# Optimization experiments

Hardware: AMD Instinct MI355X
Metric: run time of the kernel (lower is better)

Reference implementation:

```python
import jax, jax.numpy as jnp
import numpy as np

IN_DIM = 128
OUT_DIM = 128
NUM_RELS = 8
N_NODES = 50000
N_EDGES = 500000


def setup_inputs() -> dict:
    key = jax.random.key(0)
    k_x, k_ei_s, k_ei_d, k_et, k_w, k_sw = jax.random.split(key, 6)
    x = jax.random.normal(k_x, (N_NODES, IN_DIM), dtype=jnp.float32)
    src = jax.random.randint(k_ei_s, (N_EDGES,), 0, N_NODES)
    dst = jax.random.randint(k_ei_d, (N_EDGES,), 0, N_NODES)
    edge_index = jnp.stack([src, dst], axis=0).astype(jnp.int64)
    edge_type = jax.random.randint(k_et, (N_EDGES,), 0, NUM_RELS).astype(jnp.int64)
    # xavier_uniform: bound = sqrt(6/(fan_in+fan_out))
    bw = float(np.sqrt(6.0 / (IN_DIM + OUT_DIM)))
    weight = jax.random.uniform(k_w, (NUM_RELS, IN_DIM, OUT_DIM), dtype=jnp.float32, minval=-bw, maxval=bw)
    self_loop_weight = jax.random.uniform(k_sw, (IN_DIM, OUT_DIM), dtype=jnp.float32, minval=-bw, maxval=bw)
    bias = jnp.zeros((OUT_DIM,), dtype=jnp.float32)
    return {
        "x": x,
        "weight": weight,
        "self_loop_weight": self_loop_weight,
        "bias": bias,
        "edge_index": edge_index,
        "edge_type": edge_type,
        "num_entities": N_NODES,
    }


def reference(x, weight, self_loop_weight, bias, edge_index, edge_type, num_entities):
    # Relation-grouped formulation of the per-edge loop:
    # transform every node under every relation once: hr[r, n, o]
    hr = jnp.einsum("nd,rdo->rno", x, weight)
    src, dst = edge_index[0], edge_index[1]
    # per-edge message = x[src] @ weight[edge_type]  == hr[edge_type, src]
    msg = hr[edge_type, src]  # [E, out]
    agg = jax.ops.segment_sum(msg, dst, num_segments=num_entities)  # scatter-add into out[dst]
    out = agg + x @ self_loop_weight + bias
    return jax.nn.relu(out)
```

## Files before the change

### kernel.cpp

```cpp
#include <hip/hip_runtime.h>

#define IN_DIM 128
#define OUT_DIM 128
#define NUM_RELS 8
#define SCAN_ELEMS 2048

typedef unsigned short u16;
typedef u16 u16x8 __attribute__((ext_vector_type(8)));
typedef u16 u16x4 __attribute__((ext_vector_type(4)));
typedef __bf16 bf16x8 __attribute__((ext_vector_type(8)));
typedef float f32x4 __attribute__((ext_vector_type(4)));

__device__ __forceinline__ u16 f2bf(float f) {
    unsigned u = __float_as_uint(f);
    u += 0x7FFF + ((u >> 16) & 1);
    return (u16)(u >> 16);
}
__device__ __forceinline__ float bf2f(u16 h) {
    return __uint_as_float((unsigned)h << 16);
}

__global__ __launch_bounds__(256) void k_prep(
    const float* __restrict__ x, const float* __restrict__ weight,
    const float* __restrict__ slw,
    u16* __restrict__ xb, u16* __restrict__ WbT, int* __restrict__ cursor,
    int N, int BA, int BB)
{
    const int b = blockIdx.x;
    const int tid = threadIdx.x;
    if (b < BA) {
        long i = ((long)b * 256 + tid) * 4;
        if (i < (long)N * 128) {
            float4 v = *(const float4*)(x + i);
            u16x4 o;
            o[0] = f2bf(v.x); o[1] = f2bf(v.y); o[2] = f2bf(v.z); o[3] = f2bf(v.w);
            *(u16x4*)(xb + i) = o;
        }
    } else if (b < BA + BB) {
        int t = (b - BA) * 256 + tid;
        int z = t >> 12;
        int rem = t & 4095;
        int kk = rem >> 5;
        int c0 = (rem & 31) * 4;
        const float* srcp = (z < 8) ? (weight + (size_t)z * 16384 + kk * 128 + c0)
                                    : (slw + kk * 128 + c0);
        float4 v = *(const float4*)srcp;
        u16* outz = WbT + (size_t)z * 16384;
        outz[(c0 + 0) * 128 + kk] = f2bf(v.x);
        outz[(c0 + 1) * 128 + kk] = f2bf(v.y);
        outz[(c0 + 2) * 128 + kk] = f2bf(v.z);
        outz[(c0 + 3) * 128 + kk] = f2bf(v.w);
    } else {
        int j = (b - BA - BB) * 256 + tid;
        if (j < N) cursor[j] = 0;
    }
}

__global__ __launch_bounds__(256, 3) void mfma_gemm5(
    const u16* __restrict__ xb,
    const u16* __restrict__ WbT,
    const float* __restrict__ bias,
    u16* __restrict__ hr,
    int N, int ntiles)
{
    __shared__ u16 slab[4][16 * 68];

    const int tid   = threadIdx.x;
    const int z     = blockIdx.z;
    const int wv    = tid >> 6;
    const int lane  = tid & 63;
    const int q     = lane >> 4;
    const int l     = lane & 15;
    const int mbase = (wv >> 1) * 64;
    const int cbase = (wv & 1) * 64;

    const u16* Wz = WbT + (size_t)z * 16384;

    u16x8 Bf[4][4];
    #pragma unroll
    for (int nt = 0; nt < 4; ++nt) {
        const u16* colp = Wz + (cbase + nt * 16 + l) * 128;
        #pragma unroll
        for (int kc = 0; kc < 4; ++kc)
            Bf[nt][kc] = *(const u16x8*)(colp + kc * 32 + q * 8);
    }

    float bv[4];
    #pragma unroll
    for (int nt = 0; nt < 4; ++nt)
        bv[nt] = (z == 8) ? bias[cbase + nt * 16 + l] : 0.f;

    u16* slabw = &slab[wv][0];
    u16* hrz = hr + ((size_t)z * N) * 128;

    for (int tile = blockIdx.x; tile < ntiles; tile += gridDim.x) {
        const int n0 = tile * 128;

        f32x4 acc[4][4] = {};
        #pragma unroll
        for (int kc = 0; kc < 4; ++kc) {
            const int k0 = kc * 32 + q * 8;
            u16x8 a[4];
            #pragma unroll
            for (int mt = 0; mt < 4; ++mt) {
                const int row = n0 + mbase + mt * 16 + l;
                u16x8 v = {};
                if (row < N) v = *(const u16x8*)(xb + (size_t)row * 128 + k0);
                a[mt] = v;
            }
            #pragma unroll
            for (int nt = 0; nt < 4; ++nt) {
                bf16x8 b = __builtin_bit_cast(bf16x8, Bf[nt][kc]);
                #pragma unroll
                for (int mt = 0; mt < 4; ++mt) {
                    acc[mt][nt] = __builtin_amdgcn_mfma_f32_16x16x32_bf16(
                        __builtin_bit_cast(bf16x8, a[mt]), b, acc[mt][nt], 0, 0, 0);
                }
            }
        }

        #pragma unroll
        for (int mt = 0; mt < 4; ++mt) {
            #pragma unroll
            for (int nt = 0; nt < 4; ++nt) {
                const int col = nt * 16 + l;
                #pragma unroll
                for (int j = 0; j < 4; ++j)
                    slabw[(q * 4 + j) * 68 + col] = f2bf(acc[mt][nt][j] + bv[nt]);
            }
            const int srow = lane >> 3;
            const int scol = (lane & 7) * 8;
            #pragma unroll
            for (int h = 0; h < 2; ++h) {
                const int r = h * 8 + srow;
                const int grow = n0 + mbase + mt * 16 + r;
                if (grow < N) {
                    u16x8 v = *(const u16x8*)&slabw[r * 68 + scol];
                    *(u16x8*)(hrz + (size_t)grow * 128 + cbase + scol) = v;
                }
            }
        }
    }
}

__global__ __launch_bounds__(256) void k_hist(
    const int* __restrict__ dst, int* __restrict__ deg, int E)
{
    int e = blockIdx.x * blockDim.x + threadIdx.x;
    if (e < E) atomicAdd(&deg[dst[e]], 1);
}

__global__ __launch_bounds__(256) void k_scan1(
    const int* __restrict__ deg, int* __restrict__ local,
    int* __restrict__ bsum, int n)
{
    __shared__ int s[256];
    const int t = threadIdx.x;
    const int base = blockIdx.x * SCAN_ELEMS + t * 8;
    int v[8];
    int sum = 0;
    #pragma unroll
    for (int j = 0; j < 8; ++j) {
        int i = base + j;
        v[j] = (i < n) ? deg[i] : 0;
        sum += v[j];
    }
    s[t] = sum;
    __syncthreads();
    #pragma unroll
    for (int off = 1; off < 256; off <<= 1) {
        int y = (t >= off) ? s[t - off] : 0;
        __syncthreads();
        s[t] += y;
        __syncthreads();
    }
    int run = s[t] - sum;
    #pragma unroll
    for (int j = 0; j < 8; ++j) {
        int i = base + j;
        if (i < n) local[i] = run;
        run += v[j];
    }
    if (t == 255) bsum[blockIdx.x] = s[255];
}

__global__ __launch_bounds__(256) void k_scan2(
    int* __restrict__ bsum, int* __restrict__ row_ptr, int B, int n)
{
    __shared__ int s[256];
    const int t = threadIdx.x;
    int v = (t < B) ? bsum[t] : 0;
    s[t] = v;
    __syncthreads();
    #pragma unroll
    for (int off = 1; off < 256; off <<= 1) {
        int y = (t >= off) ? s[t - off] : 0;
        __syncthreads();
        s[t] += y;
        __syncthreads();
    }
    if (t < B) bsum[t] = s[t] - v;
    if (t == 255) row_ptr[n] = s[255];
}

__global__ __launch_bounds__(256) void k_scan3(
    int* __restrict__ row_ptr, const int* __restrict__ bsum,
    int* __restrict__ cursor, int n)
{
    const int t = threadIdx.x;
    const int base = blockIdx.x * SCAN_ELEMS + t * 8;
    const int off = bsum[blockIdx.x];
    #pragma unroll
    for (int j = 0; j < 8; ++j) {
        int i = base + j;
        if (i < n) {
            int val = row_ptr[i] + off;
            row_ptr[i] = val;
            cursor[i] = val;
        }
    }
}

__global__ __launch_bounds__(256) void k_fill(
    const int* __restrict__ src, const int* __restrict__ dst,
    const int* __restrict__ et, int* __restrict__ cursor,
    int* __restrict__ packed, int E)
{
    int e = blockIdx.x * blockDim.x + threadIdx.x;
    if (e >= E) return;
    int pos = atomicAdd(&cursor[dst[e]], 1);
    packed[pos] = (et[e] << 17) | src[e];
}

__global__ __launch_bounds__(256) void gather_bf16(
    const u16* __restrict__ hr,
    const u16* __restrict__ hself,
    const int* __restrict__ row_ptr, const int* __restrict__ packed,
    float* __restrict__ out, int Nn, int N)
{
    int g = blockIdx.x * 8 + (threadIdx.x >> 5);
    int lane = threadIdx.x & 31;
    if (g >= Nn) return;
    const int beg = row_ptr[g];
    const int end = row_ptr[g + 1];

    u16x4 s = *(const u16x4*)(hself + (size_t)g * 128 + lane * 4);
    float a0 = bf2f(s[0]), a1 = bf2f(s[1]), a2 = bf2f(s[2]), a3 = bf2f(s[3]);
    float b0 = 0.f, b1 = 0.f, b2 = 0.f, b3 = 0.f;
    float c0 = 0.f, c1 = 0.f, c2 = 0.f, c3 = 0.f;
    float d0 = 0.f, d1 = 0.f, d2 = 0.f, d3 = 0.f;

    const int lo = lane * 4;
    int k = beg;
    for (; k + 4 <= end; k += 4) {
        int p0 = packed[k], p1 = packed[k + 1], p2 = packed[k + 2], p3 = packed[k + 3];
        u16x4 v0 = *(const u16x4*)(hr + ((size_t)(p0 >> 17) * N + (p0 & 0x1FFFF)) * 128 + lo);
        u16x4 v1 = *(const u16x4*)(hr + ((size_t)(p1 >> 17) * N + (p1 & 0x1FFFF)) * 128 + lo);
        u16x4 v2 = *(const u16x4*)(hr + ((size_t)(p2 >> 17) * N + (p2 & 0x1FFFF)) * 128 + lo);
        u16x4 v3 = *(const u16x4*)(hr + ((size_t)(p3 >> 17) * N + (p3 & 0x1FFFF)) * 128 + lo);
        a0 += bf2f(v0[0]); a1 += bf2f(v0[1]); a2 += bf2f(v0[2]); a3 += bf2f(v0[3]);
        b0 += bf2f(v1[0]); b1 += bf2f(v1[1]); b2 += bf2f(v1[2]); b3 += bf2f(v1[3]);
        c0 += bf2f(v2[0]); c1 += bf2f(v2[1]); c2 += bf2f(v2[2]); c3 += bf2f(v2[3]);
        d0 += bf2f(v3[0]); d1 += bf2f(v3[1]); d2 += bf2f(v3[2]); d3 += bf2f(v3[3]);
    }
    for (; k < end; ++k) {
        int p = packed[k];
        u16x4 v = *(const u16x4*)(hr + ((size_t)(p >> 17) * N + (p & 0x1FFFF)) * 128 + lo);
        a0 += bf2f(v[0]); a1 += bf2f(v[1]); a2 += bf2f(v[2]); a3 += bf2f(v[3]);
    }
    a0 += b0 + c0 + d0; a1 += b1 + c1 + d1;
    a2 += b2 + c2 + d2; a3 += b3 + c3 + d3;

    float4 o = make_float4(fmaxf(a0, 0.f), fmaxf(a1, 0.f),
                           fmaxf(a2, 0.f), fmaxf(a3, 0.f));
    *(float4*)(out + (size_t)g * 128 + lane * 4) = o;
}

__global__ __launch_bounds__(256) void gemm128(
    const float* __restrict__ x, const float* __restrict__ W,
    const float* __restrict__ bias, float* __restrict__ out, int N)
{
    __shared__ float Ws[IN_DIM * OUT_DIM];
    __shared__ float xs[16][IN_DIM];

    const float* Wz = W + (size_t)blockIdx.z * IN_DIM * OUT_DIM;
    float* outz = out + (size_t)blockIdx.z * (size_t)N * OUT_DIM;

    {
        const float4* s4 = (const float4*)Wz;
        float4* d4 = (float4*)Ws;
        for (int i = threadIdx.x; i < IN_DIM * OUT_DIM / 4; i += 256)
            d4[i] = s4[i];
    }

    const int tid = threadIdx.x;
    const int nl = (tid >> 5) * 2;
    const int og = (tid & 31) * 4;

    float4 b4 = make_float4(0.f, 0.f, 0.f, 0.f);
    if (bias) b4 = *(const float4*)&bias[og];

    const int nchunks = (N + 15) / 16;
    for (int chunk = blockIdx.x; chunk < nchunks; chunk += gridDim.x) {
        const int n0 = chunk * 16;
        const int rows = min(16, N - n0);
        __syncthreads();
        {
            const float4* xsrc = (const float4*)(x + (size_t)n0 * IN_DIM);
            float4* xdst = (float4*)&xs[0][0];
            const int n4 = rows * (IN_DIM / 4);
            for (int i = tid; i < n4; i += 256) xdst[i] = xsrc[i];
        }
        __syncthreads();

        if (nl < rows) {
            float a00 = 0.f, a01 = 0.f, a02 = 0.f, a03 = 0.f;
            float a10 = 0.f, a11 = 0.f, a12 = 0.f, a13 = 0.f;
            #pragma unroll 8
            for (int d = 0; d < IN_DIM; ++d) {
                const float4 w4 = *(const float4*)&Ws[d * OUT_DIM + og];
                const float xa = xs[nl][d];
                const float xb = xs[nl + 1][d];
                a00 += xa * w4.x; a01 += xa * w4.y; a02 += xa * w4.z; a03 += xa * w4.w;
                a10 += xb * w4.x; a11 += xb * w4.y; a12 += xb * w4.z; a13 += xb * w4.w;
            }
            float4 r0 = make_float4(a00 + b4.x, a01 + b4.y, a02 + b4.z, a03 + b4.w);
            *(float4*)&outz[(size_t)(n0 + nl) * OUT_DIM + og] = r0;
            if (nl + 1 < rows) {
                float4 r1 = make_float4(a10 + b4.x, a11 + b4.y, a12 + b4.z, a13 + b4.w);
                *(float4*)&outz[(size_t)(n0 + nl + 1) * OUT_DIM + og] = r1;
            }
        }
    }
}

__global__ __launch_bounds__(256) void edge_direct(
    const float* __restrict__ x, const float* __restrict__ W,
    const int* __restrict__ src, const int* __restrict__ dst,
    const int* __restrict__ et, float* __restrict__ out, int E)
{
    long t = (long)blockIdx.x * blockDim.x + threadIdx.x;
    long e = t >> 6;
    int lane = (int)(t & 63);
    if (e >= E) return;
    int s = src[e], d = dst[e], r = et[e];
    const float* xr = x + (long)s * IN_DIM;
    float2 xv = *(const float2*)(xr + lane * 2);
    const float* Wr = W + (long)r * IN_DIM * OUT_DIM;
    const int o0 = lane * 2;
    float a0 = 0.f, a1 = 0.f;
    #pragma unroll 8
    for (int dd = 0; dd < 64; ++dd) {
        float xa = __shfl(xv.x, dd);
        float xb = __shfl(xv.y, dd);
        a0 += xa * Wr[(2 * dd) * OUT_DIM + o0]     + xb * Wr[(2 * dd + 1) * OUT_DIM + o0];
        a1 += xa * Wr[(2 * dd) * OUT_DIM + o0 + 1] + xb * Wr[(2 * dd + 1) * OUT_DIM + o0 + 1];
    }
    atomicAdd(out + (long)d * OUT_DIM + o0, a0);
    atomicAdd(out + (long)d * OUT_DIM + o0 + 1, a1);
}

__global__ __launch_bounds__(256) void relu_k(float* __restrict__ out, long n4)
{
    long i = (long)blockIdx.x * blockDim.x + threadIdx.x;
    if (i >= n4) return;
    float4 v = ((float4*)out)[i];
    v.x = fmaxf(v.x, 0.f); v.y = fmaxf(v.y, 0.f);
    v.z = fmaxf(v.z, 0.f); v.w = fmaxf(v.w, 0.f);
    ((float4*)out)[i] = v;
}

static inline size_t align256(size_t x) { return (x + 255) & ~(size_t)255; }

extern "C" void kernel_launch(void* const* d_in, const int* in_sizes, int n_in,
                              void* d_out, int out_size, void* d_ws, size_t ws_size,
                              hipStream_t stream)
{
    const float* x      = (const float*)d_in[0];
    const float* weight = (const float*)d_in[1];
    const float* slw    = (const float*)d_in[2];
    const float* bias   = (const float*)d_in[3];
    const int*   ei     = (const int*)d_in[4];
    const int*   et     = (const int*)d_in[5];

    const int N = in_sizes[0] / IN_DIM;
    const int E = in_sizes[5];
    const int* src  = ei;
    const int* dstp = ei + E;

    float* out = (float*)d_out;

    size_t off = 0;
    const size_t xb_off   = off; off += align256((size_t)N * 128 * 2);
    const size_t wb_off   = off; off += align256((size_t)9 * 128 * 128 * 2);
    const size_t hr_off   = off; off += align256((size_t)9 * N * 128 * 2);
    const size_t rp_off   = off; off += align256((size_t)(N + 1) * 4);
    const size_t cur_off  = off; off += align256((size_t)N * 4);
    const size_t pk_off   = off; off += align256((size_t)E * 4);
    const size_t bs_off   = off; off += align256(256 * 4);
    const size_t need_bf16 = off;

    const int scanB = (N + SCAN_ELEMS - 1) / SCAN_ELEMS;

    if (ws_size >= need_bf16 && N <= (1 << 17) && scanB <= 256) {
        char* base   = (char*)d_ws;
        u16* xb      = (u16*)(base + xb_off);
        u16* WbT     = (u16*)(base + wb_off);
        u16* hr      = (u16*)(base + hr_off);
        int* row_ptr = (int*)(base + rp_off);
        int* cursor  = (int*)(base + cur_off);
        int* packed  = (int*)(base + pk_off);
        int* bsum    = (int*)(base + bs_off);

        const int BA = (int)(((long)N * 128 / 4 + 255) / 256);
        const int BB = 9 * 4096 / 256;
        const int BC = (N + 255) / 256;
        k_prep<<<dim3(BA + BB + BC), 256, 0, stream>>>(
            x, weight, slw, xb, WbT, cursor, N, BA, BB);

        k_hist<<<dim3((E + 255) / 256), 256, 0, stream>>>(dstp, cursor, E);
        k_scan1<<<dim3(scanB), 256, 0, stream>>>(cursor, row_ptr, bsum, N);
        k_scan2<<<dim3(1), 256, 0, stream>>>(bsum, row_ptr, scanB, N);
        k_scan3<<<dim3(scanB), 256, 0, stream>>>(row_ptr, bsum, cursor, N);
        k_fill<<<dim3((E + 255) / 256), 256, 0, stream>>>(src, dstp, et, cursor, packed, E);

        const int ntiles = (N + 127) / 128;
        const int gx = ntiles < 56 ? ntiles : 56;
        mfma_gemm5<<<dim3(gx, 1, 9), 256, 0, stream>>>(xb, WbT, bias, hr, N, ntiles);

        gather_bf16<<<dim3((N + 7) / 8), 256, 0, stream>>>(
            hr, hr + (size_t)8 * N * 128, row_ptr, packed, out, N, N);
    } else if (ws_size >= (size_t)NUM_RELS * N * 128 * 4) {
        gemm128<<<dim3(512, 1, 1), 256, 0, stream>>>(x, slw, bias, out, N);
        long nt = (long)E * 64;
        edge_direct<<<dim3((nt + 255) / 256), 256, 0, stream>>>(x, weight, src, dstp, et, out, E);
        long n4 = (long)N * OUT_DIM / 4;
        relu_k<<<dim3((n4 + 255) / 256), 256, 0, stream>>>(out, n4);
    } else {
        gemm128<<<dim3(512, 1, 1), 256, 0, stream>>>(x, slw, bias, out, N);
        long nt = (long)E * 64;
        edge_direct<<<dim3((nt + 255) / 256), 256, 0, stream>>>(x, weight, src, dstp, et, out, E);
        long n4 = (long)N * OUT_DIM / 4;
        relu_k<<<dim3((n4 + 255) / 256), 256, 0, stream>>>(out, n4);
    }
}
```

Measured before the change: 231.8 us.

## Merge scan passes, widen gather to 16-byte loads, drop weight transpose

Several changes at once. The weight prep becomes a plain vectorized bf16 conversion with no transpose, so the GEMM now gathers its B fragments with strided scalar loads once per block. The second and third scan kernels are merged: every block redoes the small block-sum scan and applies its own offset, which removes one launch. The gather kernel moves to 16 lanes per node, each handling 8 bf16 values with 16-byte loads. The GEMM's occupancy hint drops from 3 to 2 blocks per SM.

```diff
diff --git a/kernel.cpp b/kernel.cpp
--- a/kernel.cpp
+++ b/kernel.cpp
@@ -23,7 +23,7 @@
 __global__ __launch_bounds__(256) void k_prep(
     const float* __restrict__ x, const float* __restrict__ weight,
     const float* __restrict__ slw,
-    u16* __restrict__ xb, u16* __restrict__ WbT, int* __restrict__ cursor,
+    u16* __restrict__ xb, u16* __restrict__ Wb, int* __restrict__ cursor,
     int N, int BA, int BB)
 {
     const int b = blockIdx.x;
@@ -37,28 +37,23 @@
             *(u16x4*)(xb + i) = o;
         }
     } else if (b < BA + BB) {
-        int t = (b - BA) * 256 + tid;
-        int z = t >> 12;
-        int rem = t & 4095;
-        int kk = rem >> 5;
-        int c0 = (rem & 31) * 4;
-        const float* srcp = (z < 8) ? (weight + (size_t)z * 16384 + kk * 128 + c0)
-                                    : (slw + kk * 128 + c0);
-        float4 v = *(const float4*)srcp;
-        u16* outz = WbT + (size_t)z * 16384;
-        outz[(c0 + 0) * 128 + kk] = f2bf(v.x);
-        outz[(c0 + 1) * 128 + kk] = f2bf(v.y);
-        outz[(c0 + 2) * 128 + kk] = f2bf(v.z);
-        outz[(c0 + 3) * 128 + kk] = f2bf(v.w);
+        long i = ((long)(b - BA) * 256 + tid) * 4;
+        if (i < 9L * 16384) {
+            const float* srcp = (i < 8L * 16384) ? (weight + i) : (slw + (i - 8L * 16384));
+            float4 v = *(const float4*)srcp;
+            u16x4 o;
+            o[0] = f2bf(v.x); o[1] = f2bf(v.y); o[2] = f2bf(v.z); o[3] = f2bf(v.w);
+            *(u16x4*)(Wb + i) = o;
+        }
     } else {
         int j = (b - BA - BB) * 256 + tid;
         if (j < N) cursor[j] = 0;
     }
 }
 
-__global__ __launch_bounds__(256, 3) void mfma_gemm5(
+__global__ __launch_bounds__(256, 2) void mfma_gemm2(
     const u16* __restrict__ xb,
-    const u16* __restrict__ WbT,
+    const u16* __restrict__ Wb,
     const float* __restrict__ bias,
     u16* __restrict__ hr,
     int N, int ntiles)
@@ -74,15 +69,19 @@
     const int mbase = (wv >> 1) * 64;
     const int cbase = (wv & 1) * 64;
 
-    const u16* Wz = WbT + (size_t)z * 16384;
+    const u16* Wz = Wb + (size_t)z * 128 * 128;
 
     u16x8 Bf[4][4];
     #pragma unroll
     for (int nt = 0; nt < 4; ++nt) {
-        const u16* colp = Wz + (cbase + nt * 16 + l) * 128;
+        const int col = cbase + nt * 16 + l;
         #pragma unroll
-        for (int kc = 0; kc < 4; ++kc)
-            Bf[nt][kc] = *(const u16x8*)(colp + kc * 32 + q * 8);
+        for (int kc = 0; kc < 4; ++kc) {
+            const int k0 = kc * 32 + q * 8;
+            #pragma unroll
+            for (int j = 0; j < 8; ++j)
+                Bf[nt][kc][j] = Wz[(k0 + j) * 128 + col];
+        }
     }
 
     float bv[4];
@@ -91,12 +90,12 @@
         bv[nt] = (z == 8) ? bias[cbase + nt * 16 + l] : 0.f;
 
     u16* slabw = &slab[wv][0];
-    u16* hrz = hr + ((size_t)z * N) * 128;
 
     for (int tile = blockIdx.x; tile < ntiles; tile += gridDim.x) {
         const int n0 = tile * 128;
 
         f32x4 acc[4][4] = {};
+
         #pragma unroll
         for (int kc = 0; kc < 4; ++kc) {
             const int k0 = kc * 32 + q * 8;
@@ -119,14 +118,16 @@
             }
         }
 
+        u16* hrz = hr + ((size_t)z * N) * 128;
         #pragma unroll
         for (int mt = 0; mt < 4; ++mt) {
             #pragma unroll
             for (int nt = 0; nt < 4; ++nt) {
                 const int col = nt * 16 + l;
                 #pragma unroll
-                for (int j = 0; j < 4; ++j)
+                for (int j = 0; j < 4; ++j) {
                     slabw[(q * 4 + j) * 68 + col] = f2bf(acc[mt][nt][j] + bv[nt]);
+                }
             }
             const int srow = lane >> 3;
             const int scol = (lane & 7) * 8;
@@ -184,8 +185,9 @@
     if (t == 255) bsum[blockIdx.x] = s[255];
 }
 
-__global__ __launch_bounds__(256) void k_scan2(
-    int* __restrict__ bsum, int* __restrict__ row_ptr, int B, int n)
+__global__ __launch_bounds__(256) void k_scan23(
+    int* __restrict__ row_ptr, const int* __restrict__ bsum,
+    int* __restrict__ cursor, int B, int n)
 {
     __shared__ int s[256];
     const int t = threadIdx.x;
@@ -199,26 +201,19 @@
         s[t] += y;
         __syncthreads();
     }
-    if (t < B) bsum[t] = s[t] - v;
-    if (t == 255) row_ptr[n] = s[255];
-}
-
-__global__ __launch_bounds__(256) void k_scan3(
-    int* __restrict__ row_ptr, const int* __restrict__ bsum,
-    int* __restrict__ cursor, int n)
-{
-    const int t = threadIdx.x;
+    const int myoff = (blockIdx.x == 0) ? 0 : s[blockIdx.x - 1];
+    const int total = s[255];
     const int base = blockIdx.x * SCAN_ELEMS + t * 8;
-    const int off = bsum[blockIdx.x];
     #pragma unroll
     for (int j = 0; j < 8; ++j) {
         int i = base + j;
         if (i < n) {
-            int val = row_ptr[i] + off;
+            int val = row_ptr[i] + myoff;
             row_ptr[i] = val;
             cursor[i] = val;
         }
     }
+    if (blockIdx.x == 0 && t == 0) row_ptr[n] = total;
 }
 
 __global__ __launch_bounds__(256) void k_fill(
@@ -238,42 +233,43 @@
     const int* __restrict__ row_ptr, const int* __restrict__ packed,
     float* __restrict__ out, int Nn, int N)
 {
-    int g = blockIdx.x * 8 + (threadIdx.x >> 5);
-    int lane = threadIdx.x & 31;
+    int g = blockIdx.x * 16 + (threadIdx.x >> 4);
+    int lane = threadIdx.x & 15;
     if (g >= Nn) return;
     const int beg = row_ptr[g];
     const int end = row_ptr[g + 1];
-
-    u16x4 s = *(const u16x4*)(hself + (size_t)g * 128 + lane * 4);
-    float a0 = bf2f(s[0]), a1 = bf2f(s[1]), a2 = bf2f(s[2]), a3 = bf2f(s[3]);
-    float b0 = 0.f, b1 = 0.f, b2 = 0.f, b3 = 0.f;
-    float c0 = 0.f, c1 = 0.f, c2 = 0.f, c3 = 0.f;
-    float d0 = 0.f, d1 = 0.f, d2 = 0.f, d3 = 0.f;
-
-    const int lo = lane * 4;
+    const int lo = lane * 8;
+
+    u16x8 sv = *(const u16x8*)(hself + (size_t)g * 128 + lo);
+    float a[8], b[8], c[8], d[8];
+    #pragma unroll
+    for (int j = 0; j < 8; ++j) { a[j] = bf2f(sv[j]); b[j] = 0.f; c[j] = 0.f; d[j] = 0.f; }
+
     int k = beg;
     for (; k + 4 <= end; k += 4) {
         int p0 = packed[k], p1 = packed[k + 1], p2 = packed[k + 2], p3 = packed[k + 3];
-        u16x4 v0 = *(const u16x4*)(hr + ((size_t)(p0 >> 17) * N + (p0 & 0x1FFFF)) * 128 + lo);
-        u16x4 v1 = *(const u16x4*)(hr + ((size_t)(p1 >> 17) * N + (p1 & 0x1FFFF)) * 128 + lo);
-        u16x4 v2 = *(const u16x4*)(hr + ((size_t)(p2 >> 17) * N + (p2 & 0x1FFFF)) * 128 + lo);
-        u16x4 v3 = *(const u16x4*)(hr + ((size_t)(p3 >> 17) * N + (p3 & 0x1FFFF)) * 128 + lo);
-        a0 += bf2f(v0[0]); a1 += bf2f(v0[1]); a2 += bf2f(v0[2]); a3 += bf2f(v0[3]);
-        b0 += bf2f(v1[0]); b1 += bf2f(v1[1]); b2 += bf2f(v1[2]); b3 += bf2f(v1[3]);
-        c0 += bf2f(v2[0]); c1 += bf2f(v2[1]); c2 += bf2f(v2[2]); c3 += bf2f(v2[3]);
-        d0 += bf2f(v3[0]); d1 += bf2f(v3[1]); d2 += bf2f(v3[2]); d3 += bf2f(v3[3]);
+        u16x8 v0 = *(const u16x8*)(hr + ((size_t)(p0 >> 17) * N + (p0 & 0x1FFFF)) * 128 + lo);
+        u16x8 v1 = *(const u16x8*)(hr + ((size_t)(p1 >> 17) * N + (p1 & 0x1FFFF)) * 128 + lo);
+        u16x8 v2 = *(const u16x8*)(hr + ((size_t)(p2 >> 17) * N + (p2 & 0x1FFFF)) * 128 + lo);
+        u16x8 v3 = *(const u16x8*)(hr + ((size_t)(p3 >> 17) * N + (p3 & 0x1FFFF)) * 128 + lo);
+        #pragma unroll
+        for (int j = 0; j < 8; ++j) {
+            a[j] += bf2f(v0[j]); b[j] += bf2f(v1[j]);
+            c[j] += bf2f(v2[j]); d[j] += bf2f(v3[j]);
+        }
     }
     for (; k < end; ++k) {
         int p = packed[k];
-        u16x4 v = *(const u16x4*)(hr + ((size_t)(p >> 17) * N + (p & 0x1FFFF)) * 128 + lo);
-        a0 += bf2f(v[0]); a1 += bf2f(v[1]); a2 += bf2f(v[2]); a3 += bf2f(v[3]);
-    }
-    a0 += b0 + c0 + d0; a1 += b1 + c1 + d1;
-    a2 += b2 + c2 + d2; a3 += b3 + c3 + d3;
-
-    float4 o = make_float4(fmaxf(a0, 0.f), fmaxf(a1, 0.f),
-                           fmaxf(a2, 0.f), fmaxf(a3, 0.f));
-    *(float4*)(out + (size_t)g * 128 + lane * 4) = o;
+        u16x8 v = *(const u16x8*)(hr + ((size_t)(p >> 17) * N + (p & 0x1FFFF)) * 128 + lo);
+        #pragma unroll
+        for (int j = 0; j < 8; ++j) a[j] += bf2f(v[j]);
+    }
+    #pragma unroll
+    for (int j = 0; j < 8; ++j) a[j] = fmaxf(a[j] + b[j] + c[j] + d[j], 0.f);
+
+    float* op = out + (size_t)g * 128 + lo;
+    *(float4*)op       = make_float4(a[0], a[1], a[2], a[3]);
+    *(float4*)(op + 4) = make_float4(a[4], a[5], a[6], a[7]);
 }
 
 __global__ __launch_bounds__(256) void gemm128(
@@ -405,7 +401,7 @@
     if (ws_size >= need_bf16 && N <= (1 << 17) && scanB <= 256) {
         char* base   = (char*)d_ws;
         u16* xb      = (u16*)(base + xb_off);
-        u16* WbT     = (u16*)(base + wb_off);
+        u16* Wb      = (u16*)(base + wb_off);
         u16* hr      = (u16*)(base + hr_off);
         int* row_ptr = (int*)(base + rp_off);
         int* cursor  = (int*)(base + cur_off);
@@ -413,22 +409,21 @@
         int* bsum    = (int*)(base + bs_off);
 
         const int BA = (int)(((long)N * 128 / 4 + 255) / 256);
-        const int BB = 9 * 4096 / 256;
+        const int BB = (9 * 16384 / 4 + 255) / 256;
         const int BC = (N + 255) / 256;
         k_prep<<<dim3(BA + BB + BC), 256, 0, stream>>>(
-            x, weight, slw, xb, WbT, cursor, N, BA, BB);
+            x, weight, slw, xb, Wb, cursor, N, BA, BB);
 
         k_hist<<<dim3((E + 255) / 256), 256, 0, stream>>>(dstp, cursor, E);
         k_scan1<<<dim3(scanB), 256, 0, stream>>>(cursor, row_ptr, bsum, N);
-        k_scan2<<<dim3(1), 256, 0, stream>>>(bsum, row_ptr, scanB, N);
-        k_scan3<<<dim3(scanB), 256, 0, stream>>>(row_ptr, bsum, cursor, N);
+        k_scan23<<<dim3(scanB), 256, 0, stream>>>(row_ptr, bsum, cursor, scanB, N);
         k_fill<<<dim3((E + 255) / 256), 256, 0, stream>>>(src, dstp, et, cursor, packed, E);
 
         const int ntiles = (N + 127) / 128;
         const int gx = ntiles < 56 ? ntiles : 56;
-        mfma_gemm5<<<dim3(gx, 1, 9), 256, 0, stream>>>(xb, WbT, bias, hr, N, ntiles);
-
-        gather_bf16<<<dim3((N + 7) / 8), 256, 0, stream>>>(
+        mfma_gemm2<<<dim3(gx, 1, 9), 256, 0, stream>>>(xb, Wb, bias, hr, N, ntiles);
+
+        gather_bf16<<<dim3((N + 15) / 16), 256, 0, stream>>>(
             hr, hr + (size_t)8 * N * 128, row_ptr, packed, out, N, N);
     } else if (ws_size >= (size_t)NUM_RELS * N * 128 * 4) {
         gemm128<<<dim3(512, 1, 1), 256, 0, stream>>>(x, slw, bias, out, N);
```

New measurement: 211.0 us. -9.0%, faster.
